# Kernel optimization log

Measured on AMD Instinct MI355X. Metric: run time of the kernel, lower is better.

Reference implementation:

```python
import jax, jax.numpy as jnp
import numpy as np
from jax import lax

B, C, H, W = 8, 4, 256, 256
INF = jnp.float32(1e6)  # > any possible distance on the grid; INF**2 safe in fp32


def _dist1d_to_zero(mask):
    """1D distance along the last axis to the nearest background (False) pixel.

    mask: [N, H, W] bool, True = foreground. Returns float32 [N, H, W].
    """
    def step(carry, z):  # carry, z: [N, H]
        d = jnp.where(z, carry + 1.0, 0.0)
        return d, d

    zT = jnp.moveaxis(mask, -1, 0)                      # [W, N, H]
    init = jnp.full(mask.shape[:-1], INF, jnp.float32)  # [N, H]
    _, left = lax.scan(step, init, zT)                  # scan left -> right
    _, right = lax.scan(step, init, zT, reverse=True)   # scan right -> left
    g = jnp.minimum(left, right)                        # [W, N, H]
    return jnp.moveaxis(g, 0, -1)                       # [N, H, W]


def _edt2d(mask):
    """Exact 2D Euclidean distance transform (Felzenszwalb-Huttenlocher style,
    vectorized envelope). mask: [N, H, W] bool. Returns float32 [N, H, W]."""
    g = _dist1d_to_zero(mask)   # per-row 1D distance to nearest zero
    g2 = g * g                  # [N, H, W]
    i = jnp.arange(mask.shape[-2], dtype=jnp.float32)
    dk2 = (i[:, None] - i[None, :]) ** 2  # [H, H] squared row offsets

    def combine(g2_img):  # g2_img: [H, W] -> exact squared EDT [H, W]
        # D2[i, j] = min_k ( (i - k)^2 + g(k, j)^2 )
        return jnp.min(dk2[:, :, None] + g2_img[None, :, :], axis=1)

    # lax.map keeps the [H, H, W] intermediate to one image at a time (~64 MB)
    d2 = lax.map(combine, g2)
    return jnp.sqrt(d2)


def setup_inputs() -> dict:
    key = jax.random.key(0)
    x = jax.random.randint(key, (B, C, H, W), 0, 2).astype(jnp.float32)
    return {"x": x}


def reference(x):
    # scipy edt treats any nonzero (incl. NaN) as foreground
    mask = (x != 0) | jnp.isnan(x)                    # [B, C, H, W]
    flat = mask.reshape(B * C, H, W)
    dist = _edt2d(flat).reshape(B, C, H, W)
    # positions that were NaN in the input are set back to NaN
    return jnp.where(jnp.isnan(x), jnp.nan, dist)
```

## Files before the change

### kernel.cpp

```cpp
#include <hip/hip_runtime.h>
#include <math.h>

#define NIMG 32
#define H 256
#define W 256

__global__ __launch_bounds__(256) void edt_rows(const float* __restrict__ x,
                                                float* __restrict__ g2) {
    const int lane = threadIdx.x & 63;
    const int wv   = threadIdx.x >> 6;
    const int row  = blockIdx.x * 4 + wv;

    const float4 v = reinterpret_cast<const float4*>(x + (size_t)row * W)[lane];
    const int base = lane * 4;

    bool bgs[4];
    bgs[0] = (v.x == 0.0f);
    bgs[1] = (v.y == 0.0f);
    bgs[2] = (v.z == 0.0f);
    bgs[3] = (v.w == 0.0f);

    int lanelast = -1;
    #pragma unroll
    for (int e = 0; e < 4; ++e) if (bgs[e]) lanelast = base + e;

    int s = lanelast;
    #pragma unroll
    for (int off = 1; off < 64; off <<= 1) {
        int t = __shfl_up(s, off);
        if (lane >= off) s = max(s, t);
    }
    int excl_last = __shfl_up(s, 1);
    if (lane == 0) excl_last = -1;

    const int BIG = 1 << 29;
    int lanefirst = BIG;
    #pragma unroll
    for (int e = 3; e >= 0; --e) if (bgs[e]) lanefirst = base + e;

    int s2 = lanefirst;
    #pragma unroll
    for (int off = 1; off < 64; off <<= 1) {
        int t = __shfl_down(s2, off);
        if (lane + off < 64) s2 = min(s2, t);
    }
    int excl_first = __shfl_down(s2, 1);
    if (lane == 63) excl_first = BIG;

    float dl[4], dr[4];
    int cur = excl_last;
    #pragma unroll
    for (int e = 0; e < 4; ++e) {
        int w = base + e;
        if (bgs[e]) { dl[e] = 0.0f; cur = w; }
        else        { dl[e] = (cur < 0) ? 1.0e6f : (float)(w - cur); }
    }
    int cur2 = excl_first;
    #pragma unroll
    for (int e = 3; e >= 0; --e) {
        int w = base + e;
        if (bgs[e]) { dr[e] = 0.0f; cur2 = w; }
        else        { dr[e] = (cur2 >= BIG) ? 1.0e6f : (float)(cur2 - w); }
    }

    float4 o;
    float a;
    a = fminf(dl[0], dr[0]); o.x = a * a;
    a = fminf(dl[1], dr[1]); o.y = a * a;
    a = fminf(dl[2], dr[2]); o.z = a * a;
    a = fminf(dl[3], dr[3]); o.w = a * a;
    reinterpret_cast<float4*>(g2 + (size_t)row * W)[lane] = o;
}

__global__ __launch_bounds__(256) void edt_cols(const float* __restrict__ g2,
                                                const float* __restrict__ x,
                                                float* __restrict__ out) {
    __shared__ float sg2[H * 64];

    const int b    = blockIdx.x;
    const int img  = b >> 4;
    const int rem  = b & 15;
    const int i0   = (rem >> 2) * 64;
    const int c0   = (rem & 3) * 64;

    const float* gbase = g2 + (size_t)img * (H * W) + c0;

    for (int idx = threadIdx.x; idx < H * 64; idx += 256) {
        int k = idx >> 6;
        int c = idx & 63;
        sg2[idx] = gbase[(size_t)k * W + c];
    }
    __syncthreads();

    const int c     = threadIdx.x & 63;
    const int ig    = threadIdx.x >> 6;
    const int ibase = i0 + ig * 16;

    float best[16];
    #pragma unroll
    for (int m = 0; m < 16; ++m) best[m] = 3.0e38f;

    #pragma unroll 4
    for (int k = 0; k < H; ++k) {
        float ld = sg2[k * 64 + c];
        float dk = (float)(ibase - k);
        #pragma unroll
        for (int m = 0; m < 16; ++m) {
            float diff = dk + (float)m;
            best[m] = fminf(best[m], fmaf(diff, diff, ld));
        }
    }

    const int ocol = c0 + c;
    #pragma unroll
    for (int m = 0; m < 16; ++m) {
        int i   = ibase + m;
        size_t idx = (size_t)img * (H * W) + (size_t)i * W + ocol;
        float xv = x[idx];
        out[idx] = (xv != xv) ? xv : sqrtf(best[m]);
    }
}

extern "C" void kernel_launch(void* const* d_in, const int* in_sizes, int n_in,
                              void* d_out, int out_size, void* d_ws, size_t ws_size,
                              hipStream_t stream) {
    const float* x  = (const float*)d_in[0];
    float* out      = (float*)d_out;
    float* g2       = (float*)d_ws;

    edt_rows<<<dim3((NIMG * H) / 4), dim3(256), 0, stream>>>(x, g2);

    edt_cols<<<dim3(NIMG * 16), dim3(256), 0, stream>>>(g2, x, out);
}
```

Measured before the change: 95.02 us.

## Restrict column EDT pass to local row window with exact fallback

The column pass now loads only a 96-row panel (the 64 output rows plus 16 rows on each side) into shared memory and scans that window instead of all 256 rows. If any thread's best squared distance exceeds (RWIN+1)^2, the whole block rescans every row from global memory, so the result stays exact. This cuts shared-memory fill and the inner min loop for inputs where nearby background is common. It adds a block-wide reduction, and inputs with large empty regions will pay for both scans.

Result: faster. 78.21 us (-17.7%).

```diff
diff --git a/kernel.cpp b/kernel.cpp
--- a/kernel.cpp
+++ b/kernel.cpp
@@ -4,6 +4,8 @@
 #define NIMG 32
 #define H 256
 #define W 256
+#define RWIN 16
+#define PANEL_ROWS (64 + 2*RWIN)
 
 __global__ __launch_bounds__(256) void edt_rows(const float* __restrict__ x,
                                                 float* __restrict__ g2) {
@@ -75,7 +77,7 @@
 __global__ __launch_bounds__(256) void edt_cols(const float* __restrict__ g2,
                                                 const float* __restrict__ x,
                                                 float* __restrict__ out) {
-    __shared__ float sg2[H * 64];
+    __shared__ float sg2[PANEL_ROWS * 64];
 
     const int b    = blockIdx.x;
     const int img  = b >> 4;
@@ -85,10 +87,12 @@
 
     const float* gbase = g2 + (size_t)img * (H * W) + c0;
 
-    for (int idx = threadIdx.x; idx < H * 64; idx += 256) {
-        int k = idx >> 6;
-        int c = idx & 63;
-        sg2[idx] = gbase[(size_t)k * W + c];
+    for (int idx = threadIdx.x; idx < PANEL_ROWS * 64; idx += 256) {
+        int srow = idx >> 6;
+        int c    = idx & 63;
+        int k    = i0 - RWIN + srow;
+        float vk = (k >= 0 && k < H) ? gbase[(size_t)k * W + c] : 1.0e12f;
+        sg2[idx] = vk;
     }
     __syncthreads();
 
@@ -100,14 +104,33 @@
     #pragma unroll
     for (int m = 0; m < 16; ++m) best[m] = 3.0e38f;
 
+    const int srow0 = ig * 16;
     #pragma unroll 4
-    for (int k = 0; k < H; ++k) {
-        float ld = sg2[k * 64 + c];
-        float dk = (float)(ibase - k);
+    for (int t = 0; t < 2 * RWIN + 16; ++t) {
+        float ld = sg2[(srow0 + t) * 64 + c];
+        float dt = (float)(RWIN - t);
         #pragma unroll
         for (int m = 0; m < 16; ++m) {
-            float diff = dk + (float)m;
+            float diff = dt + (float)m;
             best[m] = fminf(best[m], fmaf(diff, diff, ld));
+        }
+    }
+
+    const float thr = (float)((RWIN + 1) * (RWIN + 1));
+    bool needExt = false;
+    #pragma unroll
+    for (int m = 0; m < 16; ++m) needExt |= (best[m] > thr);
+
+    if (__syncthreads_count(needExt ? 1 : 0) != 0) {
+        #pragma unroll 4
+        for (int k = 0; k < H; ++k) {
+            float ld = gbase[(size_t)k * W + c];
+            float dk = (float)(ibase - k);
+            #pragma unroll
+            for (int m = 0; m < 16; ++m) {
+                float diff = dk + (float)m;
+                best[m] = fminf(best[m], fmaf(diff, diff, ld));
+            }
         }
     }
 
```
